# Optimization experiments

Hardware: AMD Instinct MI355X
Metric: run time of the kernel (lower is better)

The kernel has to match this reference:

```python
import jax, jax.numpy as jnp
import numpy as np

UNITS = 100000
S = 64.0
M1 = 1.0
M2 = 0.5
M3 = 0.0


def setup_inputs() -> dict:
    key = jax.random.key(0)
    k1, k2, k3 = jax.random.split(key, 3)
    inputs = jax.random.normal(k1, (512, 512), dtype=jnp.float32)
    label = jax.random.randint(k2, (512,), 0, UNITS, dtype=jnp.int64)
    # fc7 weight, init stddev 0.01 as in the original layer
    w = jax.random.normal(k3, (512, UNITS), dtype=jnp.float32) * 0.01
    return {"inputs": inputs, "label": label, "w": w}


def reference(inputs, label, w):
    # L2-normalize embeddings (rows) and weights (columns)
    emb = inputs / jnp.linalg.norm(inputs, axis=-1, keepdims=True)
    wn = w / jnp.linalg.norm(w, axis=0, keepdims=True)
    # fc7 = s * cos(theta), shape [batch, units]
    fc7 = jnp.matmul(emb * S, wn)
    # ArcFace margin branch (m1=1.0, m2=0.5, m3=0.0)
    cos_t = fc7 / S
    t = jnp.arccos(cos_t)
    if M1 != 1.0:
        t = t * M1
    if M2 > 0.0:
        t = t + M2
    body = jnp.cos(t)
    if M3 > 0.0:
        body = body - M3
    diff = body * S - fc7
    one_hot = jax.nn.one_hot(label, UNITS, dtype=fc7.dtype)
    fc7 = fc7 + one_hot * diff
    return jax.nn.softmax(fc7, axis=-1)
```

## Files before the change

### kernel.cpp

```cpp
#include <hip/hip_runtime.h>
#include <math.h>

#define UNITS 100000
#define BATCH 512
#define DIM 512
#define BN 64
#define NBLK ((UNITS + BN - 1) / BN)
#define SCALE 64.0f
#define COS_M2 0.87758256189037271612f
#define SIN_M2 0.47942553860420300027f
#define LOG2E  1.44269504088896340736f

typedef _Float16 half8 __attribute__((ext_vector_type(8)));
typedef float floatx4 __attribute__((ext_vector_type(4)));

#define PHASE_BARRIER() do { \
    asm volatile("s_waitcnt lgkmcnt(0)" ::: "memory"); \
    __builtin_amdgcn_s_barrier(); \
} while (0)

__global__ void norm_emb_k(const float* __restrict__ inp, _Float16* __restrict__ A2) {
    const int row = blockIdx.x;
    const int lane = threadIdx.x;
    const float* rp = inp + row * DIM + lane * 8;
    float v[8];
#pragma unroll
    for (int j = 0; j < 8; ++j) v[j] = rp[j];
    float ss = 0.f;
#pragma unroll
    for (int j = 0; j < 8; ++j) ss += v[j] * v[j];
#pragma unroll
    for (int off = 32; off > 0; off >>= 1) ss += __shfl_xor(ss, off);
    const float inv = SCALE / sqrtf(ss);
    half8 h;
#pragma unroll
    for (int j = 0; j < 8; ++j) h[j] = (_Float16)(v[j] * inv);
    const int idx = ((((row >> 4) * 16 + (lane >> 2)) * 64) + (row & 15) + 16 * (lane & 3)) * 8;
    *(half8*)(A2 + idx) = h;
}

template<bool HALF>
__global__ __launch_bounds__(512, 4) void gemmfused_k(
    const float* __restrict__ w, const _Float16* __restrict__ A2,
    const int* __restrict__ label,
    _Float16* __restrict__ vh, float* __restrict__ outf,
    float* __restrict__ psum, float* __restrict__ pmax) {
    __shared__ _Float16 Bt[2][512 * 8];
    __shared__ float sqred[8][64];
    __shared__ float cninv_s[64];
    __shared__ float sums_s[512];
    __shared__ float maxs_s[512];

    const int t = threadIdx.x;
    const int blk = blockIdx.x;
    const int c0 = blk * BN;
    const int w8 = t >> 6;
    const int lane = t & 63;
    const int colg = lane & 15;
    const int rowg = lane >> 4;

    const bool cval = (c0 + lane) < UNITS;
    const float* wbase = w + (cval ? (c0 + lane) : (UNITS - 1));

    float sq = 0.f;
    float rs[2][8];

    auto LOADC = [&](int ch, float* r) {
#pragma unroll
        for (int i = 0; i < 8; ++i)
            r[i] = wbase[(size_t)(ch * 64 + w8 * 8 + i) * UNITS];
    };
    auto WRITEC = [&](const float* r, int buf) {
        half8 h;
#pragma unroll
        for (int i = 0; i < 8; ++i) {
            const float x = cval ? r[i] : 0.f;
            sq += x * x;
            h[i] = (_Float16)x;
        }
        *(half8*)&Bt[buf][(w8 * 64 + lane) * 8] = h;
    };

    floatx4 acc[4][4];
#pragma unroll
    for (int mf = 0; mf < 4; ++mf)
#pragma unroll
        for (int nf = 0; nf < 4; ++nf) acc[mf][nf] = (floatx4){0.f, 0.f, 0.f, 0.f};

    auto MFMAC = [&](int ch, int buf) {
#pragma unroll
        for (int ksl = 0; ksl < 2; ++ksl) {
            half8 b[4];
#pragma unroll
            for (int nf = 0; nf < 4; ++nf)
                b[nf] = *(const half8*)&Bt[buf][((ksl * 4 + rowg) * 64 + nf * 16 + colg) * 8];
#pragma unroll
            for (int mf = 0; mf < 4; ++mf) {
                const half8 a = *(const half8*)(A2 +
                    (size_t)(((w8 * 4 + mf) * 16 + ch * 2 + ksl) * 64 + lane) * 8);
#pragma unroll
                for (int nf = 0; nf < 4; ++nf)
                    acc[mf][nf] = __builtin_amdgcn_mfma_f32_16x16x32_f16(a, b[nf], acc[mf][nf], 0, 0, 0);
            }
        }
    };

    LOADC(0, rs[0]);
    LOADC(1, rs[1]);
    WRITEC(rs[0], 0);
    PHASE_BARRIER();
#pragma unroll
    for (int ch = 0; ch < 8; ++ch) {
        if (ch + 2 < 8) LOADC(ch + 2, rs[ch & 1]);
        if (ch + 1 < 8) WRITEC(rs[1 - (ch & 1)], (ch + 1) & 1);
        MFMAC(ch, ch & 1);
        PHASE_BARRIER();
    }

    sqred[w8][lane] = sq;
    __syncthreads();
    if (t < 64) {
        float s = 0.f;
#pragma unroll
        for (int g = 0; g < 8; ++g) s += sqred[g][t];
        cninv_s[t] = rsqrtf(s);
    }
    __syncthreads();

    float cn[4];
#pragma unroll
    for (int nf = 0; nf < 4; ++nf) cn[nf] = cninv_s[nf * 16 + colg];

    _Float16* bounce = &Bt[0][0] + w8 * 1024;

#pragma unroll
    for (int mf = 0; mf < 4; ++mf) {
#pragma unroll
        for (int r = 0; r < 4; ++r) {
            const int R = w8 * 64 + mf * 16 + rowg * 4 + r;
            const int labv = label[R];
            float lg[4];
            float mx = -1e30f;
#pragma unroll
            for (int nf = 0; nf < 4; ++nf) {
                const int C = c0 + nf * 16 + colg;
                float x = acc[mf][nf][r] * cn[nf];
                if (C == labv) {
                    float cs = fminf(1.f, fmaxf(-1.f, x * (1.0f / SCALE)));
                    x = SCALE * (cs * COS_M2 - sqrtf(fmaxf(0.f, 1.f - cs * cs)) * SIN_M2);
                }
                if (C >= UNITS) x = -1e30f;
                lg[nf] = x;
                mx = fmaxf(mx, x);
            }
            mx = fmaxf(mx, __shfl_xor(mx, 1));
            mx = fmaxf(mx, __shfl_xor(mx, 2));
            mx = fmaxf(mx, __shfl_xor(mx, 4));
            mx = fmaxf(mx, __shfl_xor(mx, 8));
            float s = 0.f;
#pragma unroll
            for (int nf = 0; nf < 4; ++nf) {
                const int C = c0 + nf * 16 + colg;
                const float e = exp2f((lg[nf] - mx) * LOG2E);
                s += (C < UNITS) ? e : 0.f;
                if (HALF) bounce[(rowg * 4 + r) * 64 + nf * 16 + colg] = (_Float16)e;
                else if (C < UNITS) outf[(size_t)R * UNITS + C] = e;
            }
            s += __shfl_xor(s, 1);
            s += __shfl_xor(s, 2);
            s += __shfl_xor(s, 4);
            s += __shfl_xor(s, 8);
            if (colg == 0) { sums_s[R] = s; maxs_s[R] = mx; }
        }
        if (HALF) {
#pragma unroll
            for (int p = 0; p < 2; ++p) {
                const int row_l = p * 8 + (lane >> 3);
                const int seg = lane & 7;
                const half8 hv = *(const half8*)&bounce[row_l * 64 + seg * 8];
                const int gc = c0 + seg * 8;
                if (gc + 8 <= UNITS)
                    *(half8*)(vh + (size_t)(w8 * 64 + mf * 16 + row_l) * UNITS + gc) = hv;
            }
        }
    }

    __syncthreads();
    psum[(size_t)blk * BATCH + t] = sums_s[t];
    pmax[(size_t)blk * BATCH + t] = maxs_s[t];
}

__global__ void rowfac_k(const float* __restrict__ psum, const float* __restrict__ pmax,
                         float* __restrict__ fac) {
    const int row = blockIdx.x;
    const int lane = threadIdx.x;
    float mx = -1e30f;
    for (int b = lane; b < NBLK; b += 64) mx = fmaxf(mx, pmax[(size_t)b * BATCH + row]);
#pragma unroll
    for (int off = 32; off > 0; off >>= 1) mx = fmaxf(mx, __shfl_xor(mx, off));
    float s = 0.f;
    for (int b = lane; b < NBLK; b += 64)
        s += psum[(size_t)b * BATCH + row] * exp2f((pmax[(size_t)b * BATCH + row] - mx) * LOG2E);
#pragma unroll
    for (int off = 32; off > 0; off >>= 1) s += __shfl_xor(s, off);
    const float invS = 1.0f / s;
    for (int b = lane; b < NBLK; b += 64)
        fac[(size_t)row * NBLK + b] = exp2f((pmax[(size_t)b * BATCH + row] - mx) * LOG2E) * invS;
}

__global__ void scale_half_k(const _Float16* __restrict__ v, const float* __restrict__ fac,
                             float* __restrict__ out) {
    const int row = blockIdx.y;
    const int c = (blockIdx.x * 256 + threadIdx.x) * 8;
    if (c >= UNITS) return;
    const float f = fac[(size_t)row * NBLK + (c >> 6)];
    const half8 h = *(const half8*)(v + (size_t)row * UNITS + c);
    float4 o1, o2;
    o1.x = (float)h[0] * f; o1.y = (float)h[1] * f; o1.z = (float)h[2] * f; o1.w = (float)h[3] * f;
    o2.x = (float)h[4] * f; o2.y = (float)h[5] * f; o2.z = (float)h[6] * f; o2.w = (float)h[7] * f;
    float* op = out + (size_t)row * UNITS + c;
    *(float4*)op = o1;
    *(float4*)(op + 4) = o2;
}

__global__ void scale_f32_k(float* __restrict__ out, const float* __restrict__ fac) {
    const int row = blockIdx.y;
    const int c = (blockIdx.x * 256 + threadIdx.x) * 8;
    if (c >= UNITS) return;
    const float f = fac[(size_t)row * NBLK + (c >> 6)];
    float* op = out + (size_t)row * UNITS + c;
    float4 o1 = *(float4*)op;
    float4 o2 = *(float4*)(op + 4);
    o1.x *= f; o1.y *= f; o1.z *= f; o1.w *= f;
    o2.x *= f; o2.y *= f; o2.z *= f; o2.w *= f;
    *(float4*)op = o1;
    *(float4*)(op + 4) = o2;
}

extern "C" void kernel_launch(void* const* d_in, const int* in_sizes, int n_in,
                              void* d_out, int out_size, void* d_ws, size_t ws_size,
                              hipStream_t stream) {
    const float* inp   = (const float*)d_in[0];
    const int*   label = (const int*)d_in[1];
    const float* w     = (const float*)d_in[2];
    float* out = (float*)d_out;

    char* ws = (char*)d_ws;
    _Float16* A2 = (_Float16*)ws;
    float* psum  = (float*)(ws + (4u << 20));
    float* pmax  = (float*)(ws + (8u << 20));
    float* fac   = (float*)(ws + (12u << 20));
    _Float16* vh = (_Float16*)(ws + (16u << 20));
    const size_t need = (size_t)(16u << 20) + (size_t)BATCH * UNITS * 2;
    const bool half_path = ws_size >= need;

    norm_emb_k<<<BATCH, 64, 0, stream>>>(inp, A2);
    if (half_path)
        gemmfused_k<true><<<NBLK, 512, 0, stream>>>(w, A2, label, vh, out, psum, pmax);
    else
        gemmfused_k<false><<<NBLK, 512, 0, stream>>>(w, A2, label, vh, out, psum, pmax);
    rowfac_k<<<BATCH, 64, 0, stream>>>(psum, pmax, fac);
    dim3 sg((UNITS + 2047) / 2048, BATCH);
    if (half_path)
        scale_half_k<<<sg, 256, 0, stream>>>(vh, fac, out);
    else
        scale_f32_k<<<sg, 256, 0, stream>>>(out, fac);
}
```

Baseline: 267.2 us.

## Split batch rows across two blocks per column tile with swizzled LDS and upfront W loads

```diff
diff --git a/kernel.cpp b/kernel.cpp
--- a/kernel.cpp
+++ b/kernel.cpp
@@ -5,7 +5,8 @@
 #define BATCH 512
 #define DIM 512
 #define BN 64
-#define NBLK ((UNITS + BN - 1) / BN)
+#define BM 256
+#define NCT 1563
 #define SCALE 64.0f
 #define COS_M2 0.87758256189037271612f
 #define SIN_M2 0.47942553860420300027f
@@ -14,10 +15,7 @@
 typedef _Float16 half8 __attribute__((ext_vector_type(8)));
 typedef float floatx4 __attribute__((ext_vector_type(4)));
 
-#define PHASE_BARRIER() do { \
-    asm volatile("s_waitcnt lgkmcnt(0)" ::: "memory"); \
-    __builtin_amdgcn_s_barrier(); \
-} while (0)
+#define BSWZ(kg, col) ((((kg) * 64) + ((col) ^ ((kg) & 7))) * 8)
 
 __global__ void norm_emb_k(const float* __restrict__ inp, _Float16* __restrict__ A2) {
     const int row = blockIdx.x;
@@ -40,84 +38,109 @@
 }
 
 template<bool HALF>
-__global__ __launch_bounds__(512, 4) void gemmfused_k(
+__global__ __launch_bounds__(512, 3) void gemmfused_k(
     const float* __restrict__ w, const _Float16* __restrict__ A2,
     const int* __restrict__ label,
     _Float16* __restrict__ vh, float* __restrict__ outf,
     float* __restrict__ psum, float* __restrict__ pmax) {
-    __shared__ _Float16 Bt[2][512 * 8];
+    __shared__ _Float16 Bt[16384];
     __shared__ float sqred[8][64];
     __shared__ float cninv_s[64];
-    __shared__ float sums_s[512];
-    __shared__ float maxs_s[512];
+    __shared__ float sums_s[BM];
+    __shared__ float maxs_s[BM];
 
     const int t = threadIdx.x;
-    const int blk = blockIdx.x;
-    const int c0 = blk * BN;
+    const int ctile = blockIdx.x >> 1;
+    const int half = blockIdx.x & 1;
+    const int c0 = ctile * BN;
     const int w8 = t >> 6;
     const int lane = t & 63;
     const int colg = lane & 15;
     const int rowg = lane >> 4;
-
-    const bool cval = (c0 + lane) < UNITS;
-    const float* wbase = w + (cval ? (c0 + lane) : (UNITS - 1));
-
-    float sq = 0.f;
-    float rs[2][8];
-
-    auto LOADC = [&](int ch, float* r) {
-#pragma unroll
-        for (int i = 0; i < 8; ++i)
-            r[i] = wbase[(size_t)(ch * 64 + w8 * 8 + i) * UNITS];
-    };
-    auto WRITEC = [&](const float* r, int buf) {
-        half8 h;
-#pragma unroll
-        for (int i = 0; i < 8; ++i) {
-            const float x = cval ? r[i] : 0.f;
-            sq += x * x;
-            h[i] = (_Float16)x;
-        }
-        *(half8*)&Bt[buf][(w8 * 64 + lane) * 8] = h;
-    };
-
-    floatx4 acc[4][4];
-#pragma unroll
-    for (int mf = 0; mf < 4; ++mf)
+    const int q = t & 15;
+    const int kr0 = t >> 4;
+
+    const bool cval = (c0 + 4 * q) < UNITS;
+    const float* wp = w + (size_t)kr0 * UNITS + (cval ? (c0 + 4 * q) : 0);
+
+    floatx4 st[16];
+#pragma unroll
+    for (int i = 0; i < 16; ++i)
+        st[i] = *(const floatx4*)(wp + (size_t)i * 32 * UNITS);
+
+    float sq[4] = {0.f, 0.f, 0.f, 0.f};
+
+#pragma unroll
+    for (int i = 0; i < 8; ++i) {
+        const int krl = i * 32 + kr0;
+#pragma unroll
+        for (int e = 0; e < 4; ++e) {
+            const float x = cval ? st[i][e] : 0.f;
+            sq[e] += x * x;
+            Bt[BSWZ(krl >> 3, 4 * q + e) + (krl & 7)] = (_Float16)x;
+        }
+    }
+    __syncthreads();
+
+    floatx4 acc[2][4];
+#pragma unroll
+    for (int mf = 0; mf < 2; ++mf)
 #pragma unroll
         for (int nf = 0; nf < 4; ++nf) acc[mf][nf] = (floatx4){0.f, 0.f, 0.f, 0.f};
 
-    auto MFMAC = [&](int ch, int buf) {
-#pragma unroll
-        for (int ksl = 0; ksl < 2; ++ksl) {
+    const _Float16* Aw = A2 + (size_t)(half * 16 + w8 * 2) * 8192 + lane * 8;
+
+#pragma unroll
+    for (int kc = 0; kc < 2; ++kc) {
+        half8 ap[2][2];
+#pragma unroll
+        for (int mf = 0; mf < 2; ++mf) {
+            ap[0][mf] = *(const half8*)(Aw + mf * 8192 + (kc * 8 + 0) * 512);
+            ap[1][mf] = *(const half8*)(Aw + mf * 8192 + (kc * 8 + 1) * 512);
+        }
+#pragma unroll
+        for (int ks = 0; ks < 8; ++ks) {
             half8 b[4];
 #pragma unroll
             for (int nf = 0; nf < 4; ++nf)
-                b[nf] = *(const half8*)&Bt[buf][((ksl * 4 + rowg) * 64 + nf * 16 + colg) * 8];
-#pragma unroll
-            for (int mf = 0; mf < 4; ++mf) {
-                const half8 a = *(const half8*)(A2 +
-                    (size_t)(((w8 * 4 + mf) * 16 + ch * 2 + ksl) * 64 + lane) * 8);
-#pragma unroll
-                for (int nf = 0; nf < 4; ++nf)
-                    acc[mf][nf] = __builtin_amdgcn_mfma_f32_16x16x32_f16(a, b[nf], acc[mf][nf], 0, 0, 0);
-            }
-        }
-    };
-
-    LOADC(0, rs[0]);
-    LOADC(1, rs[1]);
-    WRITEC(rs[0], 0);
-    PHASE_BARRIER();
-#pragma unroll
-    for (int ch = 0; ch < 8; ++ch) {
-        if (ch + 2 < 8) LOADC(ch + 2, rs[ch & 1]);
-        if (ch + 1 < 8) WRITEC(rs[1 - (ch & 1)], (ch + 1) & 1);
-        MFMAC(ch, ch & 1);
-        PHASE_BARRIER();
-    }
-
-    sqred[w8][lane] = sq;
+                b[nf] = *(const half8*)&Bt[BSWZ(ks * 4 + rowg, nf * 16 + colg)];
+            const half8 a0 = ap[ks & 1][0];
+            const half8 a1 = ap[ks & 1][1];
+            if (ks + 2 < 8) {
+                ap[ks & 1][0] = *(const half8*)(Aw + 0 * 8192 + (kc * 8 + ks + 2) * 512);
+                ap[ks & 1][1] = *(const half8*)(Aw + 1 * 8192 + (kc * 8 + ks + 2) * 512);
+            }
+#pragma unroll
+            for (int nf = 0; nf < 4; ++nf) {
+                acc[0][nf] = __builtin_amdgcn_mfma_f32_16x16x32_f16(a0, b[nf], acc[0][nf], 0, 0, 0);
+                acc[1][nf] = __builtin_amdgcn_mfma_f32_16x16x32_f16(a1, b[nf], acc[1][nf], 0, 0, 0);
+            }
+        }
+        if (kc == 0) {
+            __syncthreads();
+#pragma unroll
+            for (int i = 8; i < 16; ++i) {
+                const int krl = (i - 8) * 32 + kr0;
+#pragma unroll
+                for (int e = 0; e < 4; ++e) {
+                    const float x = cval ? st[i][e] : 0.f;
+                    sq[e] += x * x;
+                    Bt[BSWZ(krl >> 3, 4 * q + e) + (krl & 7)] = (_Float16)x;
+                }
+            }
+            __syncthreads();
+        }
+    }
+
+#pragma unroll
+    for (int e = 0; e < 4; ++e) {
+        sq[e] += __shfl_xor(sq[e], 16);
+        sq[e] += __shfl_xor(sq[e], 32);
+    }
+    if (lane < 16) {
+#pragma unroll
+        for (int e = 0; e < 4; ++e) sqred[w8][4 * lane + e] = sq[e];
+    }
     __syncthreads();
     if (t < 64) {
         float s = 0.f;
@@ -131,14 +154,15 @@
 #pragma unroll
     for (int nf = 0; nf < 4; ++nf) cn[nf] = cninv_s[nf * 16 + colg];
 
-    _Float16* bounce = &Bt[0][0] + w8 * 1024;
-
-#pragma unroll
-    for (int mf = 0; mf < 4; ++mf) {
+    _Float16* bounce = Bt + w8 * 2048;
+
+#pragma unroll
+    for (int mf = 0; mf < 2; ++mf) {
 #pragma unroll
         for (int r = 0; r < 4; ++r) {
-            const int R = w8 * 64 + mf * 16 + rowg * 4 + r;
-            const int labv = label[R];
+            const int Rl = w8 * 32 + mf * 16 + rowg * 4 + r;
+            const int Rg = half * BM + Rl;
+            const int labv = label[Rg];
             float lg[4];
             float mx = -1e30f;
 #pragma unroll
@@ -164,48 +188,55 @@
                 const float e = exp2f((lg[nf] - mx) * LOG2E);
                 s += (C < UNITS) ? e : 0.f;
                 if (HALF) bounce[(rowg * 4 + r) * 64 + nf * 16 + colg] = (_Float16)e;
-                else if (C < UNITS) outf[(size_t)R * UNITS + C] = e;
+                else if (C < UNITS) outf[(size_t)Rg * UNITS + C] = e;
             }
             s += __shfl_xor(s, 1);
             s += __shfl_xor(s, 2);
             s += __shfl_xor(s, 4);
             s += __shfl_xor(s, 8);
-            if (colg == 0) { sums_s[R] = s; maxs_s[R] = mx; }
+            if (colg == 0) { sums_s[Rl] = s; maxs_s[Rl] = mx; }
         }
         if (HALF) {
 #pragma unroll
             for (int p = 0; p < 2; ++p) {
                 const int row_l = p * 8 + (lane >> 3);
                 const int seg = lane & 7;
+                const int gc = c0 + seg * 8;
                 const half8 hv = *(const half8*)&bounce[row_l * 64 + seg * 8];
-                const int gc = c0 + seg * 8;
                 if (gc + 8 <= UNITS)
-                    *(half8*)(vh + (size_t)(w8 * 64 + mf * 16 + row_l) * UNITS + gc) = hv;
-            }
-        }
-    }
-
-    __syncthreads();
-    psum[(size_t)blk * BATCH + t] = sums_s[t];
-    pmax[(size_t)blk * BATCH + t] = maxs_s[t];
+                    *(half8*)(vh + (size_t)(half * BM + w8 * 32 + mf * 16 + row_l) * UNITS + gc) = hv;
+            }
+        }
+    }
+
+    __syncthreads();
+    if (t < BM) {
+        psum[(size_t)blockIdx.x * BM + t] = sums_s[t];
+        pmax[(size_t)blockIdx.x * BM + t] = maxs_s[t];
+    }
 }
 
 __global__ void rowfac_k(const float* __restrict__ psum, const float* __restrict__ pmax,
                          float* __restrict__ fac) {
     const int row = blockIdx.x;
     const int lane = threadIdx.x;
+    const int hb = row >> 8;
+    const int rl = row & 255;
     float mx = -1e30f;
-    for (int b = lane; b < NBLK; b += 64) mx = fmaxf(mx, pmax[(size_t)b * BATCH + row]);
+    for (int b = lane; b < NCT; b += 64)
+        mx = fmaxf(mx, pmax[(size_t)(b * 2 + hb) * BM + rl]);
 #pragma unroll
     for (int off = 32; off > 0; off >>= 1) mx = fmaxf(mx, __shfl_xor(mx, off));
     float s = 0.f;
-    for (int b = lane; b < NBLK; b += 64)
-        s += psum[(size_t)b * BATCH + row] * exp2f((pmax[(size_t)b * BATCH + row] - mx) * LOG2E);
+    for (int b = lane; b < NCT; b += 64)
+        s += psum[(size_t)(b * 2 + hb) * BM + rl] *
+             exp2f((pmax[(size_t)(b * 2 + hb) * BM + rl] - mx) * LOG2E);
 #pragma unroll
     for (int off = 32; off > 0; off >>= 1) s += __shfl_xor(s, off);
     const float invS = 1.0f / s;
-    for (int b = lane; b < NBLK; b += 64)
-        fac[(size_t)row * NBLK + b] = exp2f((pmax[(size_t)b * BATCH + row] - mx) * LOG2E) * invS;
+    for (int b = lane; b < NCT; b += 64)
+        fac[(size_t)row * NCT + b] =
+            exp2f((pmax[(size_t)(b * 2 + hb) * BM + rl] - mx) * LOG2E) * invS;
 }
 
 __global__ void scale_half_k(const _Float16* __restrict__ v, const float* __restrict__ fac,
@@ -213,7 +244,7 @@
     const int row = blockIdx.y;
     const int c = (blockIdx.x * 256 + threadIdx.x) * 8;
     if (c >= UNITS) return;
-    const float f = fac[(size_t)row * NBLK + (c >> 6)];
+    const float f = fac[(size_t)row * NCT + (c >> 6)];
     const half8 h = *(const half8*)(v + (size_t)row * UNITS + c);
     float4 o1, o2;
     o1.x = (float)h[0] * f; o1.y = (float)h[1] * f; o1.z = (float)h[2] * f; o1.w = (float)h[3] * f;
@@ -227,7 +258,7 @@
     const int row = blockIdx.y;
     const int c = (blockIdx.x * 256 + threadIdx.x) * 8;
     if (c >= UNITS) return;
-    const float f = fac[(size_t)row * NBLK + (c >> 6)];
+    const float f = fac[(size_t)row * NCT + (c >> 6)];
     float* op = out + (size_t)row * UNITS + c;
     float4 o1 = *(float4*)op;
     float4 o2 = *(float4*)(op + 4);
@@ -256,9 +287,9 @@
 
     norm_emb_k<<<BATCH, 64, 0, stream>>>(inp, A2);
     if (half_path)
-        gemmfused_k<true><<<NBLK, 512, 0, stream>>>(w, A2, label, vh, out, psum, pmax);
+        gemmfused_k<true><<<NCT * 2, 512, 0, stream>>>(w, A2, label, vh, out, psum, pmax);
     else
-        gemmfused_k<false><<<NBLK, 512, 0, stream>>>(w, A2, label, vh, out, psum, pmax);
+        gemmfused_k<false><<<NCT * 2, 512, 0, stream>>>(w, A2, label, vh, out, psum, pmax);
     rowfac_k<<<BATCH, 64, 0, stream>>>(psum, pmax, fac);
     dim3 sg((UNITS + 2047) / 2048, BATCH);
     if (half_path)
```

Result: slower. 365.6 us (+36.8%).
